# Optimization experiments

Hardware: AMD Instinct MI355X
Metric: run time of the kernel (lower is better)

## Reference

```python
import jax, jax.numpy as jnp
import numpy as np

NUM_HEADS = 12

def _pe(L, d):
    # standard sinusoidal positional encoding, shape (1, L, d)
    pos = jnp.arange(L, dtype=jnp.float32)[:, None]
    i = jnp.arange(d)[None, :]
    angle = pos / jnp.power(10000.0, (2 * (i // 2)).astype(jnp.float32) / d)
    pe = jnp.where(i % 2 == 0, jnp.sin(angle), jnp.cos(angle))
    return pe[None]

def _ln(x, scale, bias, eps=1e-5):
    m = x.mean(-1, keepdims=True)
    v = ((x - m) ** 2).mean(-1, keepdims=True)
    return (x - m) / jnp.sqrt(v + eps) * scale + bias

def setup_inputs() -> dict:
    key = jax.random.key(0)
    ks = jax.random.split(key, 8)
    D = 768
    s = 0.02
    return {
        "x": jax.random.normal(ks[0], (8, D, 32, 32), jnp.float32),
        "context_token": jax.random.normal(ks[1], (1, 1, D), jnp.float32),
        "register_tokens": jax.random.normal(ks[2], (1, 4, D), jnp.float32),
        "in_proj_w": jax.random.normal(ks[3], (3 * D, D), jnp.float32) * s,
        "in_proj_b": jnp.zeros((3 * D,), jnp.float32),
        "out_proj_w": jax.random.normal(ks[4], (D, D), jnp.float32) * s,
        "out_proj_b": jnp.zeros((D,), jnp.float32),
        "ln1_s": jnp.ones((D,), jnp.float32),
        "ln1_b": jnp.zeros((D,), jnp.float32),
        "ln2_s": jnp.ones((D,), jnp.float32),
        "ln2_b": jnp.zeros((D,), jnp.float32),
        "ffn_w1": jax.random.normal(ks[5], (4 * D, D), jnp.float32) * s,
        "ffn_b1": jnp.zeros((4 * D,), jnp.float32),
        "ffn_w2": jax.random.normal(ks[6], (D, 4 * D), jnp.float32) * s,
        "ffn_b2": jnp.zeros((D,), jnp.float32),
    }

def reference(x, context_token, register_tokens, in_proj_w, in_proj_b,
              out_proj_w, out_proj_b, ln1_s, ln1_b, ln2_s, ln2_b,
              ffn_w1, ffn_b1, ffn_w2, ffn_b2):
    B, d, h, w = x.shape
    N = h * w
    R = register_tokens.shape[1]
    G = 1 + R  # global tokens: context + registers
    nh = NUM_HEADS
    dh = d // nh
    # (B, N, d)
    x_flat = x.reshape(B, d, N).transpose(0, 2, 1)
    tokens = jnp.concatenate([
        jnp.broadcast_to(context_token, (B, 1, d)),
        jnp.broadcast_to(register_tokens, (B, R, d)),
    ], axis=1)
    tokens = tokens + _pe(G, d)
    xwt = _ln(jnp.concatenate([tokens, x_flat], axis=1), ln1_s, ln1_b)
    S = G + N
    # MultiheadAttention (eval mode, dropout off): fused in-projection
    qkv = xwt @ in_proj_w.T + in_proj_b
    q, k, v = jnp.split(qkv, 3, axis=-1)
    to_heads = lambda t: t.reshape(B, S, nh, dh).transpose(0, 2, 1, 3)
    q, k, v = to_heads(q), to_heads(k), to_heads(v)
    scores = jnp.einsum('bhqd,bhkd->bhqk', q, k) / np.float32(np.sqrt(dh))
    # mask (True = disallowed): feature rows (>=G) cannot attend to global cols (<G);
    # global rows attend everything; feature-feature block allowed.
    row_feat = jnp.arange(S) >= G
    col_glob = jnp.arange(S) < G
    disallowed = row_feat[:, None] & col_glob[None, :]
    scores = jnp.where(disallowed, -jnp.inf, scores)
    attn = jax.nn.softmax(scores, axis=-1)
    o = jnp.einsum('bhqk,bhkd->bhqd', attn, v).transpose(0, 2, 1, 3).reshape(B, S, d)
    o = o @ out_proj_w.T + out_proj_b
    y = o + xwt
    ff = jax.nn.gelu(_ln(y, ln2_s, ln2_b) @ ffn_w1.T + ffn_b1, approximate=False) @ ffn_w2.T + ffn_b2
    y = y + ff
    context_out = y[:, 0:1, :]
    register_out = y[:, 1:G, :]
    feature_out = y[:, G:, :].transpose(0, 2, 1).reshape(B, d, h, w)
    return feature_out, context_out, register_out
```

## Files before the change

kernel.cpp:

```cpp
#include <hip/hip_runtime.h>
#include <hip/hip_bf16.h>
#include <cmath>

typedef unsigned short u16;
typedef __bf16 bf16x8 __attribute__((ext_vector_type(8)));
typedef float floatx4 __attribute__((ext_vector_type(4)));

#define SQ 1029
#define DM 768
#define NH 12
#define SQP 1088
#define SSC 0.18033688011112042f

#define GLD16(gp, lp) __builtin_amdgcn_global_load_lds( \
    (const __attribute__((address_space(1))) unsigned int*)(gp), \
    (__attribute__((address_space(3))) unsigned int*)(lp), 16, 0, 0)

#define OFF_WQKV ((size_t)0)
#define OFF_WOUT ((size_t)3538944)
#define OFF_W1   ((size_t)4718592)
#define OFF_W2   ((size_t)9437184)
#define OFF_XF   ((size_t)14155776)
#define OFF_XWT  ((size_t)26800128)
#define OFF_QKV  ((size_t)39444480)
#define OFF_VT   ((size_t)77783040)
#define OFF_Y    ((size_t)91152384)
#define OFF_BQ   ((size_t)103796736)

__device__ __forceinline__ float bf2f(u16 u) {
  unsigned int x = ((unsigned int)u) << 16;
  float f; __builtin_memcpy(&f, &x, 4); return f;
}
__device__ __forceinline__ u16 f2bf(float f) {
  unsigned int x; __builtin_memcpy(&x, &f, 4);
  x = (x + 0x7fffu + ((x >> 16) & 1u)) >> 16;
  return (u16)x;
}
__device__ __forceinline__ unsigned int pk_bf16(float a, float b) {
  __hip_bfloat162 h = __float22bfloat162_rn(make_float2(a, b));
  unsigned int u; __builtin_memcpy(&u, &h, 4); return u;
}

__device__ __forceinline__ void blockReduce2(float& s1, float& s2) {
  #pragma unroll
  for (int o = 32; o > 0; o >>= 1) { s1 += __shfl_xor(s1, o); s2 += __shfl_xor(s2, o); }
  __shared__ float t1[4], t2[4];
  const int w = threadIdx.x >> 6;
  if ((threadIdx.x & 63) == 0) { t1[w] = s1; t2[w] = s2; }
  __syncthreads();
  s1 = t1[0] + t1[1] + t1[2] + t1[3];
  s2 = t2[0] + t2[1] + t2[2] + t2[3];
}

__global__ __launch_bounds__(256) void convw_all(
    const float* __restrict__ a, const float* __restrict__ b,
    const float* __restrict__ c, const float* __restrict__ d,
    const float* __restrict__ bq, u16* __restrict__ dst, float* __restrict__ bqs) {
  int i = blockIdx.x * 256 + threadIdx.x;
  if (i >= 1770048) return;
  if (i >= 1769472) {
    const int off = i - 1769472;
    float4 v = ((const float4*)bq)[off];
    if (off < 192) { v.x *= SSC; v.y *= SSC; v.z *= SSC; v.w *= SSC; }
    ((float4*)bqs)[off] = v;
    return;
  }
  const float* src; int off;
  if (i < 442368)       { src = a; off = i; }
  else if (i < 589824)  { src = b; off = i - 442368; }
  else if (i < 1179648) { src = c; off = i - 589824; }
  else                  { src = d; off = i - 1179648; }
  float4 v = ((const float4*)src)[off];
  if (i < 147456) { v.x *= SSC; v.y *= SSC; v.z *= SSC; v.w *= SSC; }
  ushort4 o; o.x = f2bf(v.x); o.y = f2bf(v.y); o.z = f2bf(v.z); o.w = f2bf(v.w);
  ((ushort4*)dst)[i] = o;
}

__global__ __launch_bounds__(256) void build_tok(
    const float* __restrict__ ctx, const float* __restrict__ regt,
    const float* __restrict__ g, const float* __restrict__ be, u16* __restrict__ xwt) {
  const int row = blockIdx.x;
  const int b = row / 5, s = row % 5;
  const int tid = threadIdx.x;
  float v[3];
  #pragma unroll
  for (int i = 0; i < 3; ++i) {
    const int c = tid + i * 256;
    float tok = (s == 0) ? ctx[c] : regt[(s - 1) * DM + c];
    float e = (float)(2 * (c / 2)) * (1.0f / 768.0f);
    float ang = (float)s / powf(10000.0f, e);
    v[i] = tok + ((c & 1) ? cosf(ang) : sinf(ang));
  }
  float s1 = v[0] + v[1] + v[2];
  float s2 = v[0] * v[0] + v[1] * v[1] + v[2] * v[2];
  blockReduce2(s1, s2);
  const float mean = s1 * (1.0f / 768.0f);
  const float var = s2 * (1.0f / 768.0f) - mean * mean;
  const float rs = rsqrtf(fmaxf(var, 0.0f) + 1e-5f);
  #pragma unroll
  for (int i = 0; i < 3; ++i) {
    const int c = tid + i * 256;
    xwt[((size_t)b * SQ + s) * DM + c] = f2bf((v[i] - mean) * rs * g[c] + be[c]);
  }
}

__global__ __launch_bounds__(256) void ln1_fused(
    const float* __restrict__ x, const float* __restrict__ g, const float* __restrict__ be,
    u16* __restrict__ xwt) {
  __shared__ u16 XT[32][772];
  const int b = blockIdx.x >> 5, st = blockIdx.x & 31;
  const int tid = threadIdx.x;
  const int i2 = tid & 15, cj = tid >> 4;
  const int n0 = st * 32;
  #pragma unroll 4
  for (int ct = 0; ct < 48; ++ct) {
    const int c = ct * 16 + cj;
    const float2 v = *(const float2*)&x[((size_t)b * 768 + c) * 1024 + n0 + i2 * 2];
    XT[i2 * 2][c]     = f2bf(v.x);
    XT[i2 * 2 + 1][c] = f2bf(v.y);
  }
  __syncthreads();
  const int wave = tid >> 6, lane = tid & 63;
  float gr[12], br[12];
  #pragma unroll
  for (int k = 0; k < 12; ++k) { gr[k] = g[lane + k * 64]; br[k] = be[lane + k * 64]; }
  #pragma unroll
  for (int rr = 0; rr < 8; ++rr) {
    const int row = wave * 8 + rr;
    float v[12];
    float s1 = 0.f, s2 = 0.f;
    #pragma unroll
    for (int k = 0; k < 12; ++k) {
      v[k] = bf2f(XT[row][lane + k * 64]);
      s1 += v[k]; s2 += v[k] * v[k];
    }
    #pragma unroll
    for (int o = 32; o > 0; o >>= 1) { s1 += __shfl_xor(s1, o); s2 += __shfl_xor(s2, o); }
    const float mean = s1 * (1.0f / 768.0f);
    const float var = s2 * (1.0f / 768.0f) - mean * mean;
    const float rs = rsqrtf(fmaxf(var, 0.0f) + 1e-5f);
    u16* dst = xwt + ((size_t)b * SQ + 5 + n0 + row) * DM;
    #pragma unroll
    for (int k = 0; k < 12; ++k)
      dst[lane + k * 64] = f2bf((v[k] - mean) * rs * gr[k] + br[k]);
  }
}

__global__ __launch_bounds__(256) void ln2k(
    const u16* __restrict__ y, const float* __restrict__ g, const float* __restrict__ be,
    u16* __restrict__ out) {
  const int row = blockIdx.x;
  const int tid = threadIdx.x;
  float v[3];
  #pragma unroll
  for (int i = 0; i < 3; ++i) v[i] = bf2f(y[(size_t)row * DM + tid + i * 256]);
  float s1 = v[0] + v[1] + v[2];
  float s2 = v[0] * v[0] + v[1] * v[1] + v[2] * v[2];
  blockReduce2(s1, s2);
  const float mean = s1 * (1.0f / 768.0f);
  const float var = s2 * (1.0f / 768.0f) - mean * mean;
  const float rs = rsqrtf(fmaxf(var, 0.0f) + 1e-5f);
  #pragma unroll
  for (int i = 0; i < 3; ++i) {
    const int c = tid + i * 256;
    out[(size_t)row * DM + c] = f2bf((v[i] - mean) * rs * g[c] + be[c]);
  }
}

template<int EPI, int K, int NB>
__global__ __launch_bounds__(256) void gemmk(
    const u16* __restrict__ A, const u16* __restrict__ W, const float* __restrict__ bias,
    const u16* __restrict__ res, u16* __restrict__ out, int M) {
  constexpr int N = NB * 128;
  __shared__ u16 SM[16384];
  u16* Asm = SM;
  u16* Bsm = SM + 8192;
  const int tid = threadIdx.x, wave = tid >> 6, lane = tid & 63, quad = lane >> 4, l16 = lane & 15;
  const int lin = blockIdx.x;
  constexpr int FULL = 64 * NB;
  int mb, nb;
  if (lin < FULL) { const int g = lin / (8 * NB); const int r = lin - g * 8 * NB; mb = g * 8 + (r & 7); nb = r >> 3; }
  else { mb = 64; nb = lin - FULL; }
  const int m0 = mb * 128, n0 = nb * 128;
  const int wm = wave & 1, wn = wave >> 1;

  const u16* Ap[4]; const u16* Wp[4]; u16* la[4]; u16* lb[4];
  #pragma unroll
  for (int it = 0; it < 4; ++it) {
    const int c = it * 256 + tid;
    const int row = c >> 3, gch = (c & 7) ^ (row & 7);
    Ap[it] = A + (size_t)min(m0 + row, M - 1) * K + gch * 8;
    Wp[it] = W + (size_t)(n0 + row) * K + gch * 8;
    la[it] = Asm + c * 8;
    lb[it] = Bsm + c * 8;
  }

  floatx4 acc[4][4];
  #pragma unroll
  for (int i = 0; i < 4; ++i)
    #pragma unroll
    for (int j = 0; j < 4; ++j) { floatx4 z = {0.f, 0.f, 0.f, 0.f}; acc[i][j] = z; }

  const int ch0 = (quad ^ (l16 & 7)) << 3;
  const int ch1 = ((4 + quad) ^ (l16 & 7)) << 3;

  #pragma unroll 1
  for (int ko = 0; ko < K / 768; ++ko) {
    #pragma unroll
    for (int ki = 0; ki < 768; ki += 64) {
      __syncthreads();
      #pragma unroll
      for (int it = 0; it < 4; ++it) GLD16(Ap[it] + ki, la[it]);
      #pragma unroll
      for (int it = 0; it < 4; ++it) GLD16(Wp[it] + ki, lb[it]);
      __syncthreads();
      #pragma unroll
      for (int kk = 0; kk < 2; ++kk) {
        const int ch = kk ? ch1 : ch0;
        bf16x8 a[4], b[4];
        #pragma unroll
        for (int i = 0; i < 4; ++i) a[i] = *(const bf16x8*)&Asm[(wm * 64 + i * 16 + l16) * 64 + ch];
        #pragma unroll
        for (int j = 0; j < 4; ++j) b[j] = *(const bf16x8*)&Bsm[(wn * 64 + j * 16 + l16) * 64 + ch];
        #pragma unroll
        for (int i = 0; i < 4; ++i)
          #pragma unroll
          for (int j = 0; j < 4; ++j)
            acc[i][j] = __builtin_amdgcn_mfma_f32_16x16x32_bf16(b[j], a[i], acc[i][j], 0, 0, 0);
      }
    }
    if (K > 768) {
      #pragma unroll
      for (int it = 0; it < 4; ++it) { Ap[it] += 768; Wp[it] += 768; }
    }
  }

  #pragma unroll
  for (int j = 0; j < 4; ++j) {
    const float4 b4 = *(const float4*)(bias + n0 + wn * 64 + j * 16 + quad * 4);
    #pragma unroll
    for (int i = 0; i < 4; ++i) {
      acc[i][j][0] += b4.x; acc[i][j][1] += b4.y; acc[i][j][2] += b4.z; acc[i][j][3] += b4.w;
    }
  }
  if constexpr (EPI == 2) {
    #pragma unroll
    for (int i = 0; i < 4; ++i)
      #pragma unroll
      for (int j = 0; j < 4; ++j)
        #pragma unroll
        for (int r = 0; r < 4; ++r) {
          const float v = acc[i][j][r];
          acc[i][j][r] = v / (1.0f + exp2f(-2.3022221f * (v + 0.044715f * v * v * v)));
        }
  }
  __syncthreads();
  u16* Ep = SM + wave * 2304;
  #pragma unroll
  for (int h = 0; h < 2; ++h) {
    #pragma unroll
    for (int i2 = 0; i2 < 2; ++i2) {
      const int i = h * 2 + i2;
      #pragma unroll
      for (int j = 0; j < 4; ++j) {
        uint2 w;
        w.x = pk_bf16(acc[i][j][0], acc[i][j][1]);
        w.y = pk_bf16(acc[i][j][2], acc[i][j][3]);
        *(uint2*)&Ep[(i2 * 16 + l16) * 72 + j * 16 + quad * 4] = w;
      }
    }
    #pragma unroll
    for (int s = 0; s < 4; ++s) {
      const int lrow = s * 8 + (lane >> 3);
      const int gm = m0 + wm * 64 + h * 32 + lrow;
      const int gn = n0 + wn * 64 + (lane & 7) * 8;
      uint4 lv = *(const uint4*)&Ep[lrow * 72 + (lane & 7) * 8];
      if constexpr (EPI == 1 || EPI == 3) {
        const uint4 rv = *(const uint4*)(res + (size_t)min(gm, M - 1) * N + gn);
        const unsigned* lp = &lv.x; const unsigned* rp = &rv.x;
        uint4 ov; unsigned* op = &ov.x;
        #pragma unroll
        for (int d = 0; d < 4; ++d) {
          const float a0 = bf2f((u16)(lp[d] & 0xffffu)) + bf2f((u16)(rp[d] & 0xffffu));
          const float a1 = bf2f((u16)(lp[d] >> 16)) + bf2f((u16)(rp[d] >> 16));
          op[d] = pk_bf16(a0, a1);
        }
        lv = ov;
      }
      if (gm < M) *(uint4*)(out + (size_t)gm * N + gn) = lv;
    }
  }
}

__global__ __launch_bounds__(256) void vtrans(const u16* __restrict__ qkv, u16* __restrict__ vt) {
  __shared__ u16 t[32][33];
  const int bh = blockIdx.x, st = blockIdx.y, dt = blockIdx.z;
  const int bq = bh / NH, hh = bh % NH;
  u16* vd = vt + (size_t)bh * 64 * SQP;
  const int i = threadIdx.x, jj = threadIdx.y;
  #pragma unroll
  for (int kk = 0; kk < 4; ++kk) {
    int j = jj + kk * 8;
    t[j][i] = qkv[(size_t)(bq * SQ + st * 32 + j) * 2304 + 1536 + hh * 64 + dt * 32 + i];
  }
  __syncthreads();
  #pragma unroll
  for (int kk = 0; kk < 4; ++kk) {
    int j = jj + kk * 8;
    vd[(size_t)(dt * 32 + j) * SQP + st * 32 + i] = t[i][j];
  }
}

__global__ __launch_bounds__(256) void attn_flash(
    const u16* __restrict__ qkv, const u16* __restrict__ vt, u16* __restrict__ out) {
  const int bh = blockIdx.x, qt = blockIdx.y;
  const int b = bh / NH, h = bh % NH;
  const int tid = threadIdx.x, wave = tid >> 6, lane = tid & 63, quad = lane >> 4, l16 = lane & 15;
  __shared__ u16 Qs[4096], Ks[4096], VTs[4096];
  __shared__ u16 Ps[64 * 72];
  const int q0 = qt * 64;
  const u16* qk = qkv + (size_t)b * SQ * 2304 + h * 64;
  const u16* vslab = vt + (size_t)bh * 64 * SQP;
  const int c0 = tid, c1 = tid + 256;
  const int r0 = c0 >> 3, q0c = (c0 & 7) ^ (r0 & 7);
  const int r1 = c1 >> 3, q1c = (c1 & 7) ^ (r1 & 7);
  u16* L0Q = Qs + wave * 512;  u16* L1Q = Qs + 2048 + wave * 512;
  u16* L0K = Ks + wave * 512;  u16* L1K = Ks + 2048 + wave * 512;
  u16* L0V = VTs + wave * 512; u16* L1V = VTs + 2048 + wave * 512;

  GLD16(qk + (size_t)(q0 + r0) * 2304 + q0c * 8, L0Q);
  GLD16(qk + (size_t)(q0 + r1) * 2304 + q1c * 8, L1Q);

  floatx4 Oa[4];
  #pragma unroll
  for (int nt = 0; nt < 4; ++nt) { floatx4 z = {0.f, 0.f, 0.f, 0.f}; Oa[nt] = z; }
  float l_acc = 0.f;
  const int qrow = wave * 16 + l16;
  const bool qfeat = (q0 + qrow >= 5);
  bf16x8 qf0, qf1;

  for (int t = 0; t < 17; ++t) {
    const int k0 = t * 64;
    __syncthreads();
    GLD16(qk + 768 + (size_t)(k0 + r0) * 2304 + q0c * 8, L0K);
    GLD16(qk + 768 + (size_t)(k0 + r1) * 2304 + q1c * 8, L1K);
    GLD16(vslab + (size_t)r0 * SQP + k0 + q0c * 8, L0V);
    GLD16(vslab + (size_t)r1 * SQP + k0 + q1c * 8, L1V);
    __syncthreads();

    if (t == 0) {
      qf0 = *(const bf16x8*)&Qs[qrow * 64 + ((quad ^ (qrow & 7)) << 3)];
      qf1 = *(const bf16x8*)&Qs[qrow * 64 + (((4 + quad) ^ (qrow & 7)) << 3)];
    }

    floatx4 st[4];
    #pragma unroll
    for (int mt = 0; mt < 4; ++mt) { floatx4 z = {0.f, 0.f, 0.f, 0.f}; st[mt] = z; }
    #pragma unroll
    for (int kk = 0; kk < 2; ++kk) {
      const bf16x8 qf = kk ? qf1 : qf0;
      #pragma unroll
      for (int mt = 0; mt < 4; ++mt) {
        const int krow = mt * 16 + l16;
        bf16x8 kf = *(const bf16x8*)&Ks[krow * 64 + (((kk * 4 + quad) ^ (krow & 7)) << 3)];
        st[mt] = __builtin_amdgcn_mfma_f32_16x16x32_bf16(kf, qf, st[mt], 0, 0, 0);
      }
    }

    if (t == 16) {
      float p[4];
      #pragma unroll
      for (int r = 0; r < 4; ++r) {
        float pv = exp2f(st[0][r]);
        p[r] = (quad * 4 + r < 5) ? pv : 0.f;
      }
      l_acc += (p[0] + p[1]) + (p[2] + p[3]);
      uint2 w;
      w.x = pk_bf16(p[0], p[1]);
      w.y = pk_bf16(p[2], p[3]);
      *(uint2*)&Ps[qrow * 72 + quad * 4] = w;
      const uint2 zz = {0u, 0u};
      #pragma unroll
      for (int mt = 1; mt < 4; ++mt) *(uint2*)&Ps[qrow * 72 + mt * 16 + quad * 4] = zz;
    } else if (t == 0) {
      #pragma unroll
      for (int mt = 0; mt < 4; ++mt) {
        float p[4];
        #pragma unroll
        for (int r = 0; r < 4; ++r) {
          float pv = exp2f(st[mt][r]);
          if (mt == 0) pv = (qfeat && (quad * 4 + r < 5)) ? 0.f : pv;
          p[r] = pv;
        }
        l_acc += (p[0] + p[1]) + (p[2] + p[3]);
        uint2 w;
        w.x = pk_bf16(p[0], p[1]);
        w.y = pk_bf16(p[2], p[3]);
        *(uint2*)&Ps[qrow * 72 + mt * 16 + quad * 4] = w;
      }
    } else {
      #pragma unroll
      for (int mt = 0; mt < 4; ++mt) {
        float p[4];
        #pragma unroll
        for (int r = 0; r < 4; ++r) p[r] = exp2f(st[mt][r]);
        l_acc += (p[0] + p[1]) + (p[2] + p[3]);
        uint2 w;
        w.x = pk_bf16(p[0], p[1]);
        w.y = pk_bf16(p[2], p[3]);
        *(uint2*)&Ps[qrow * 72 + mt * 16 + quad * 4] = w;
      }
    }

    auto pv_step = [&](int kk) {
      bf16x8 pf = *(const bf16x8*)&Ps[qrow * 72 + kk * 32 + quad * 8];
      #pragma unroll
      for (int nt = 0; nt < 4; ++nt) {
        const int brow = nt * 16 + l16;
        bf16x8 bb = *(const bf16x8*)&VTs[brow * 64 + (((kk * 4 + quad) ^ (brow & 7)) << 3)];
        Oa[nt] = __builtin_amdgcn_mfma_f32_16x16x32_bf16(pf, bb, Oa[nt], 0, 0, 0);
      }
    };
    pv_step(0);
    if (t != 16) pv_step(1);
  }

  float lt = l_acc;
  lt += __shfl_xor(lt, 16);
  lt += __shfl_xor(lt, 32);
  lt = fmaxf(lt, 1e-30f);
  #pragma unroll
  for (int nt = 0; nt < 4; ++nt)
    #pragma unroll
    for (int r = 0; r < 4; ++r) {
      const int qo = quad * 4 + r;
      const float lr = __shfl(lt, (lane & 48) | qo);
      const int qg2 = q0 + wave * 16 + qo;
      if (qg2 < SQ)
        out[((size_t)b * SQ + qg2) * DM + h * 64 + nt * 16 + l16] = f2bf(Oa[nt][r] / lr);
    }
}

__global__ __launch_bounds__(256) void transpose_out(const u16* __restrict__ yf, float* __restrict__ out) {
  __shared__ u16 tile[32][33];
  const int b = blockIdx.x, nt = blockIdx.y, ct = blockIdx.z;
  const int i = threadIdx.x, jj = threadIdx.y;
  #pragma unroll
  for (int kk = 0; kk < 4; ++kk) {
    int j = jj + kk * 8;
    tile[j][i] = yf[((size_t)b * SQ + 5 + nt * 32 + j) * DM + ct * 32 + i];
  }
  __syncthreads();
  #pragma unroll
  for (int kk = 0; kk < 4; ++kk) {
    int j = jj + kk * 8;
    out[((size_t)b * 768 + ct * 32 + j) * 1024 + nt * 32 + i] = bf2f(tile[i][j]);
  }
}

__global__ __launch_bounds__(256) void out_small(const u16* __restrict__ yf, float* __restrict__ out) {
  const int idx = blockIdx.x * 256 + threadIdx.x;
  if (idx >= 8 * 5 * DM) return;
  const int b = idx / (5 * DM);
  const int r = idx % (5 * DM);
  const int s = r / DM, c = r % DM;
  const float v = bf2f(yf[((size_t)b * SQ + s) * DM + c]);
  if (s == 0) out[(size_t)6291456 + (size_t)b * DM + c] = v;
  else out[(size_t)6291456 + 6144 + ((size_t)b * 4 + (s - 1)) * DM + c] = v;
}

extern "C" void kernel_launch(void* const* d_in, const int* in_sizes, int n_in,
                              void* d_out, int out_size, void* d_ws, size_t ws_size,
                              hipStream_t stream) {
  const float* x    = (const float*)d_in[0];
  const float* ctx  = (const float*)d_in[1];
  const float* regt = (const float*)d_in[2];
  const float* wqkv = (const float*)d_in[3];
  const float* bqkv = (const float*)d_in[4];
  const float* wout = (const float*)d_in[5];
  const float* bout = (const float*)d_in[6];
  const float* ln1s = (const float*)d_in[7];
  const float* ln1b = (const float*)d_in[8];
  const float* ln2s = (const float*)d_in[9];
  const float* ln2b = (const float*)d_in[10];
  const float* w1   = (const float*)d_in[11];
  const float* b1   = (const float*)d_in[12];
  const float* w2   = (const float*)d_in[13];
  const float* b2   = (const float*)d_in[14];

  char* ws = (char*)d_ws;
  u16* wb_all = (u16*)(ws + OFF_WQKV);
  u16* wqkv_b = (u16*)(ws + OFF_WQKV);
  u16* wout_b = (u16*)(ws + OFF_WOUT);
  u16* w1_b   = (u16*)(ws + OFF_W1);
  u16* w2_b   = (u16*)(ws + OFF_W2);
  u16* xwt    = (u16*)(ws + OFF_XWT);
  u16* qkv    = (u16*)(ws + OFF_QKV);
  u16* vtb    = (u16*)(ws + OFF_VT);
  u16* yb     = (u16*)(ws + OFF_Y);
  float* bqs  = (float*)(ws + OFF_BQ);
  u16* attnb  = (u16*)(ws + OFF_XF);
  u16* ynorm  = (u16*)(ws + OFF_XF);
  u16* h1     = (u16*)(ws + OFF_QKV);
  u16* yfin   = (u16*)(ws + OFF_XWT);
  float* outp = (float*)d_out;

  convw_all   <<<6915, 256, 0, stream>>>(wqkv, wout, w1, w2, bqkv, wb_all, bqs);
  build_tok   <<<40, 256, 0, stream>>>(ctx, regt, ln1s, ln1b, xwt);
  ln1_fused   <<<256, 256, 0, stream>>>(x, ln1s, ln1b, xwt);
  gemmk<0, 768, 18><<<65 * 18, 256, 0, stream>>>(xwt, wqkv_b, bqs, nullptr, qkv, 8232);
  vtrans      <<<dim3(96, 34, 2), dim3(32, 8), 0, stream>>>(qkv, vtb);
  attn_flash  <<<dim3(96, 17), 256, 0, stream>>>(qkv, vtb, attnb);
  gemmk<1, 768, 6><<<65 * 6, 256, 0, stream>>>(attnb, wout_b, bout, xwt, yb, 8232);
  ln2k        <<<8232, 256, 0, stream>>>(yb, ln2s, ln2b, ynorm);
  gemmk<2, 768, 24><<<65 * 24, 256, 0, stream>>>(ynorm, w1_b, b1, nullptr, h1, 8232);
  gemmk<3, 3072, 6><<<65 * 6, 256, 0, stream>>>(h1, w2_b, b2, yb, yfin, 8232);
  transpose_out<<<dim3(8, 32, 24), dim3(32, 8), 0, stream>>>(yfin, outp);
  out_small   <<<120, 256, 0, stream>>>(yfin, outp);
}
```

Before: 395.3 us.

## Add 128-thread GEMM variant for QKV/FFN1 and merge small launch kernels

Adds a gemmw kernel that uses 128 threads per block, with each wave computing a 128x64 tile (8x4 MFMA fragments), and uses it for the QKV and FFN1 GEMMs. The aim is more register-level reuse per wave and possibly better occupancy. It also folds build_tok into ln1_fused and out_small into transpose_out, cutting two kernel launches. The larger per-wave accumulator raises register pressure, and the new kernel has no double buffering, so load latency stays exposed.

```diff
diff --git a/kernel.cpp b/kernel.cpp
--- a/kernel.cpp
+++ b/kernel.cpp
@@ -76,40 +76,38 @@
   ((ushort4*)dst)[i] = o;
 }
 
-__global__ __launch_bounds__(256) void build_tok(
-    const float* __restrict__ ctx, const float* __restrict__ regt,
+__global__ __launch_bounds__(256) void ln1_fused(
+    const float* __restrict__ x, const float* __restrict__ ctx, const float* __restrict__ regt,
     const float* __restrict__ g, const float* __restrict__ be, u16* __restrict__ xwt) {
-  const int row = blockIdx.x;
-  const int b = row / 5, s = row % 5;
+  const int bx = blockIdx.x;
   const int tid = threadIdx.x;
-  float v[3];
-  #pragma unroll
-  for (int i = 0; i < 3; ++i) {
-    const int c = tid + i * 256;
-    float tok = (s == 0) ? ctx[c] : regt[(s - 1) * DM + c];
-    float e = (float)(2 * (c / 2)) * (1.0f / 768.0f);
-    float ang = (float)s / powf(10000.0f, e);
-    v[i] = tok + ((c & 1) ? cosf(ang) : sinf(ang));
-  }
-  float s1 = v[0] + v[1] + v[2];
-  float s2 = v[0] * v[0] + v[1] * v[1] + v[2] * v[2];
-  blockReduce2(s1, s2);
-  const float mean = s1 * (1.0f / 768.0f);
-  const float var = s2 * (1.0f / 768.0f) - mean * mean;
-  const float rs = rsqrtf(fmaxf(var, 0.0f) + 1e-5f);
-  #pragma unroll
-  for (int i = 0; i < 3; ++i) {
-    const int c = tid + i * 256;
-    xwt[((size_t)b * SQ + s) * DM + c] = f2bf((v[i] - mean) * rs * g[c] + be[c]);
-  }
-}
-
-__global__ __launch_bounds__(256) void ln1_fused(
-    const float* __restrict__ x, const float* __restrict__ g, const float* __restrict__ be,
-    u16* __restrict__ xwt) {
+  if (bx >= 256) {
+    const int row = bx - 256;
+    const int b = row / 5, s = row % 5;
+    float v[3];
+    #pragma unroll
+    for (int i = 0; i < 3; ++i) {
+      const int c = tid + i * 256;
+      float tok = (s == 0) ? ctx[c] : regt[(s - 1) * DM + c];
+      float e = (float)(2 * (c / 2)) * (1.0f / 768.0f);
+      float ang = (float)s / powf(10000.0f, e);
+      v[i] = tok + ((c & 1) ? cosf(ang) : sinf(ang));
+    }
+    float s1 = v[0] + v[1] + v[2];
+    float s2 = v[0] * v[0] + v[1] * v[1] + v[2] * v[2];
+    blockReduce2(s1, s2);
+    const float mean = s1 * (1.0f / 768.0f);
+    const float var = s2 * (1.0f / 768.0f) - mean * mean;
+    const float rs = rsqrtf(fmaxf(var, 0.0f) + 1e-5f);
+    #pragma unroll
+    for (int i = 0; i < 3; ++i) {
+      const int c = tid + i * 256;
+      xwt[((size_t)b * SQ + s) * DM + c] = f2bf((v[i] - mean) * rs * g[c] + be[c]);
+    }
+    return;
+  }
   __shared__ u16 XT[32][772];
-  const int b = blockIdx.x >> 5, st = blockIdx.x & 31;
-  const int tid = threadIdx.x;
+  const int b = bx >> 5, st = bx & 31;
   const int i2 = tid & 15, cj = tid >> 4;
   const int n0 = st * 32;
   #pragma unroll 4
@@ -292,6 +290,128 @@
   }
 }
 
+template<int EPI, int K, int NB>
+__global__ __launch_bounds__(128, 2) void gemmw(
+    const u16* __restrict__ A, const u16* __restrict__ W, const float* __restrict__ bias,
+    const u16* __restrict__ res, u16* __restrict__ out, int M) {
+  constexpr int N = NB * 128;
+  __shared__ u16 SM[16384];
+  u16* Asm = SM;
+  u16* Bsm = SM + 8192;
+  const int tid = threadIdx.x, wave = tid >> 6, lane = tid & 63, quad = lane >> 4, l16 = lane & 15;
+  const int lin = blockIdx.x;
+  constexpr int FULL = 64 * NB;
+  int mb, nb;
+  if (lin < FULL) { const int g = lin / (8 * NB); const int r = lin - g * 8 * NB; mb = g * 8 + (r & 7); nb = r >> 3; }
+  else { mb = 64; nb = lin - FULL; }
+  const int m0 = mb * 128, n0 = nb * 128;
+
+  const u16* Ap[8]; const u16* Wp[8];
+  #pragma unroll
+  for (int it = 0; it < 8; ++it) {
+    const int row = it * 16 + (tid >> 3);
+    const int gch = (tid & 7) ^ (row & 7);
+    Ap[it] = A + (size_t)min(m0 + row, M - 1) * K + gch * 8;
+    Wp[it] = W + (size_t)(n0 + row) * K + gch * 8;
+  }
+
+  floatx4 acc[8][4];
+  #pragma unroll
+  for (int i = 0; i < 8; ++i)
+    #pragma unroll
+    for (int j = 0; j < 4; ++j) { floatx4 z = {0.f, 0.f, 0.f, 0.f}; acc[i][j] = z; }
+
+  const int ch0 = (quad ^ (l16 & 7)) << 3;
+  const int ch1 = ((4 + quad) ^ (l16 & 7)) << 3;
+
+  #pragma unroll 1
+  for (int ko = 0; ko < K / 768; ++ko) {
+    #pragma unroll
+    for (int ki = 0; ki < 768; ki += 64) {
+      __syncthreads();
+      #pragma unroll
+      for (int it = 0; it < 8; ++it) GLD16(Ap[it] + ki, (char*)SM + (it * 128 + tid) * 16);
+      #pragma unroll
+      for (int it = 0; it < 8; ++it) GLD16(Wp[it] + ki, (char*)SM + 16384 + (it * 128 + tid) * 16);
+      __syncthreads();
+      #pragma unroll
+      for (int kk = 0; kk < 2; ++kk) {
+        const int ch = kk ? ch1 : ch0;
+        bf16x8 a[8], b[4];
+        #pragma unroll
+        for (int i = 0; i < 8; ++i) a[i] = *(const bf16x8*)&Asm[(i * 16 + l16) * 64 + ch];
+        #pragma unroll
+        for (int j = 0; j < 4; ++j) b[j] = *(const bf16x8*)&Bsm[(wave * 64 + j * 16 + l16) * 64 + ch];
+        #pragma unroll
+        for (int i = 0; i < 8; ++i)
+          #pragma unroll
+          for (int j = 0; j < 4; ++j)
+            acc[i][j] = __builtin_amdgcn_mfma_f32_16x16x32_bf16(b[j], a[i], acc[i][j], 0, 0, 0);
+      }
+    }
+    if (K > 768) {
+      #pragma unroll
+      for (int it = 0; it < 8; ++it) { Ap[it] += 768; Wp[it] += 768; }
+    }
+  }
+
+  #pragma unroll
+  for (int j = 0; j < 4; ++j) {
+    const float4 b4 = *(const float4*)(bias + n0 + wave * 64 + j * 16 + quad * 4);
+    #pragma unroll
+    for (int i = 0; i < 8; ++i) {
+      acc[i][j][0] += b4.x; acc[i][j][1] += b4.y; acc[i][j][2] += b4.z; acc[i][j][3] += b4.w;
+    }
+  }
+  if constexpr (EPI == 2) {
+    #pragma unroll
+    for (int i = 0; i < 8; ++i)
+      #pragma unroll
+      for (int j = 0; j < 4; ++j)
+        #pragma unroll
+        for (int r = 0; r < 4; ++r) {
+          const float v = acc[i][j][r];
+          acc[i][j][r] = v / (1.0f + exp2f(-2.3022221f * (v + 0.044715f * v * v * v)));
+        }
+  }
+  __syncthreads();
+  u16* Ep = SM + wave * 2304;
+  #pragma unroll
+  for (int g = 0; g < 4; ++g) {
+    #pragma unroll
+    for (int i2 = 0; i2 < 2; ++i2) {
+      const int i = g * 2 + i2;
+      #pragma unroll
+      for (int j = 0; j < 4; ++j) {
+        uint2 w;
+        w.x = pk_bf16(acc[i][j][0], acc[i][j][1]);
+        w.y = pk_bf16(acc[i][j][2], acc[i][j][3]);
+        *(uint2*)&Ep[(i2 * 16 + l16) * 72 + j * 16 + quad * 4] = w;
+      }
+    }
+    #pragma unroll
+    for (int s = 0; s < 4; ++s) {
+      const int lrow = s * 8 + (lane >> 3);
+      const int gm = m0 + g * 32 + lrow;
+      const int gn = n0 + wave * 64 + (lane & 7) * 8;
+      uint4 lv = *(const uint4*)&Ep[lrow * 72 + (lane & 7) * 8];
+      if constexpr (EPI == 1 || EPI == 3) {
+        const uint4 rv = *(const uint4*)(res + (size_t)min(gm, M - 1) * N + gn);
+        const unsigned* lp = &lv.x; const unsigned* rp = &rv.x;
+        uint4 ov; unsigned* op = &ov.x;
+        #pragma unroll
+        for (int d = 0; d < 4; ++d) {
+          const float a0 = bf2f((u16)(lp[d] & 0xffffu)) + bf2f((u16)(rp[d] & 0xffffu));
+          const float a1 = bf2f((u16)(lp[d] >> 16)) + bf2f((u16)(rp[d] >> 16));
+          op[d] = pk_bf16(a0, a1);
+        }
+        lv = ov;
+      }
+      if (gm < M) *(uint4*)(out + (size_t)gm * N + gn) = lv;
+    }
+  }
+}
+
 __global__ __launch_bounds__(256) void vtrans(const u16* __restrict__ qkv, u16* __restrict__ vt) {
   __shared__ u16 t[32][33];
   const int bh = blockIdx.x, st = blockIdx.y, dt = blockIdx.z;
@@ -442,9 +562,22 @@
 }
 
 __global__ __launch_bounds__(256) void transpose_out(const u16* __restrict__ yf, float* __restrict__ out) {
+  const int bx = blockIdx.x;
+  const int tid = threadIdx.x;
+  if (bx >= 6144) {
+    const int idx = (bx - 6144) * 256 + tid;
+    if (idx >= 8 * 5 * DM) return;
+    const int b = idx / (5 * DM);
+    const int r = idx % (5 * DM);
+    const int s = r / DM, c = r % DM;
+    const float v = bf2f(yf[((size_t)b * SQ + s) * DM + c]);
+    if (s == 0) out[(size_t)6291456 + (size_t)b * DM + c] = v;
+    else out[(size_t)6291456 + 6144 + ((size_t)b * 4 + (s - 1)) * DM + c] = v;
+    return;
+  }
   __shared__ u16 tile[32][33];
-  const int b = blockIdx.x, nt = blockIdx.y, ct = blockIdx.z;
-  const int i = threadIdx.x, jj = threadIdx.y;
+  const int b = bx / 768, rr = bx % 768, nt = rr / 24, ct = rr % 24;
+  const int i = tid & 31, jj = tid >> 5;
   #pragma unroll
   for (int kk = 0; kk < 4; ++kk) {
     int j = jj + kk * 8;
@@ -456,17 +589,6 @@
     int j = jj + kk * 8;
     out[((size_t)b * 768 + ct * 32 + j) * 1024 + nt * 32 + i] = bf2f(tile[i][j]);
   }
-}
-
-__global__ __launch_bounds__(256) void out_small(const u16* __restrict__ yf, float* __restrict__ out) {
-  const int idx = blockIdx.x * 256 + threadIdx.x;
-  if (idx >= 8 * 5 * DM) return;
-  const int b = idx / (5 * DM);
-  const int r = idx % (5 * DM);
-  const int s = r / DM, c = r % DM;
-  const float v = bf2f(yf[((size_t)b * SQ + s) * DM + c]);
-  if (s == 0) out[(size_t)6291456 + (size_t)b * DM + c] = v;
-  else out[(size_t)6291456 + 6144 + ((size_t)b * 4 + (s - 1)) * DM + c] = v;
 }
 
 extern "C" void kernel_launch(void* const* d_in, const int* in_sizes, int n_in,
@@ -506,15 +628,13 @@
   float* outp = (float*)d_out;
 
   convw_all   <<<6915, 256, 0, stream>>>(wqkv, wout, w1, w2, bqkv, wb_all, bqs);
-  build_tok   <<<40, 256, 0, stream>>>(ctx, regt, ln1s, ln1b, xwt);
-  ln1_fused   <<<256, 256, 0, stream>>>(x, ln1s, ln1b, xwt);
-  gemmk<0, 768, 18><<<65 * 18, 256, 0, stream>>>(xwt, wqkv_b, bqs, nullptr, qkv, 8232);
+  ln1_fused   <<<296, 256, 0, stream>>>(x, ctx, regt, ln1s, ln1b, xwt);
+  gemmw<0, 768, 18><<<65 * 18, 128, 0, stream>>>(xwt, wqkv_b, bqs, nullptr, qkv, 8232);
   vtrans      <<<dim3(96, 34, 2), dim3(32, 8), 0, stream>>>(qkv, vtb);
   attn_flash  <<<dim3(96, 17), 256, 0, stream>>>(qkv, vtb, attnb);
   gemmk<1, 768, 6><<<65 * 6, 256, 0, stream>>>(attnb, wout_b, bout, xwt, yb, 8232);
   ln2k        <<<8232, 256, 0, stream>>>(yb, ln2s, ln2b, ynorm);
-  gemmk<2, 768, 24><<<65 * 24, 256, 0, stream>>>(ynorm, w1_b, b1, nullptr, h1, 8232);
+  gemmw<2, 768, 24><<<65 * 24, 128, 0, stream>>>(ynorm, w1_b, b1, nullptr, h1, 8232);
   gemmk<3, 3072, 6><<<65 * 6, 256, 0, stream>>>(h1, w2_b, b2, yb, yfin, 8232);
-  transpose_out<<<dim3(8, 32, 24), dim3(32, 8), 0, stream>>>(yfin, outp);
-  out_small   <<<120, 256, 0, stream>>>(yfin, outp);
-}
+  transpose_out<<<6264, 256, 0, stream>>>(yfin, outp);
+}
```

Result: faster. 384.8 us (-2.7%).
